# Performance work log

Hardware: AMD Instinct MI355X
Metric: run time of the kernel (lower is better)

The kernel has to match this reference:

```python
import jax, jax.numpy as jnp
import numpy as np

NEG_SLOPE = 0.2  # DenseGATConv default negative_slope


def _add_self_loops(adj):
    n = adj.shape[-1]
    idx = jnp.arange(n)
    return adj.at[:, idx, idx].set(1.0)


def dense_gat_conv(x, adj, W, att_src, att_dst, bias, concat):
    """PyG DenseGATConv forward (eval mode, add_loop=True).
    x: [B,N,F], adj: [B,N,N] (0/1), W: [F,H*C], att_*: [H,C], bias: [H*C] or [C]."""
    B, N, _ = x.shape
    H, C = att_src.shape
    h = (x @ W).reshape(B, N, H, C)                     # projected features
    a_src = jnp.einsum('bnhc,hc->bnh', h, att_src)      # [B,N,H]
    a_dst = jnp.einsum('bnhc,hc->bnh', h, att_dst)      # [B,N,H]
    # alpha[b,i,j,h] = a_src[b,j,h] + a_dst[b,i,h]
    alpha = a_src[:, None, :, :] + a_dst[:, :, None, :]  # [B,N,N,H]
    alpha = jax.nn.leaky_relu(alpha, NEG_SLOPE)
    adj = _add_self_loops(adj)
    alpha = jnp.where(adj[..., None] == 0, -jnp.inf, alpha)
    alpha = jax.nn.softmax(alpha, axis=2)               # softmax over sources j
    out = jnp.einsum('bijh,bjhc->bihc', alpha, h)       # [B,N,H,C]
    out = out.reshape(B, N, H * C) if concat else out.mean(axis=2)
    return out + bias


def setup_inputs() -> dict:
    key = jax.random.key(0)
    ks = jax.random.split(key, 10)
    B, N, F, H, C, NC = 1, 4096, 512, 8, 64, 16
    x = jax.random.normal(ks[0], (B, N, F), dtype=jnp.float32)
    adj = (jax.random.uniform(ks[1], (B, N, N)) < 0.01).astype(jnp.float32)
    s1 = 1.0 / np.sqrt(F)
    s2 = 1.0 / np.sqrt(H * C)
    return {
        'x': x,
        'adj': adj,
        'W1': jax.random.normal(ks[2], (F, H * C), dtype=jnp.float32) * s1,
        'att_src1': jax.random.normal(ks[3], (H, C), dtype=jnp.float32) * s1,
        'att_dst1': jax.random.normal(ks[4], (H, C), dtype=jnp.float32) * s1,
        'b1': jnp.zeros((H * C,), dtype=jnp.float32),
        'W2': jax.random.normal(ks[5], (H * C, NC), dtype=jnp.float32) * s2,
        'att_src2': jax.random.normal(ks[6], (1, NC), dtype=jnp.float32) * s2,
        'att_dst2': jax.random.normal(ks[7], (1, NC), dtype=jnp.float32) * s2,
        'b2': jnp.zeros((NC,), dtype=jnp.float32),
    }


def reference(x, adj, W1, att_src1, att_dst1, b1, W2, att_src2, att_dst2, b2):
    # eval mode: all dropout(p=0.6) layers are identity
    h = dense_gat_conv(x, adj, W1, att_src1, att_dst1, b1, concat=True)
    h = jax.nn.elu(h)
    out = dense_gat_conv(h, adj, W2, att_src2, att_dst2, b2, concat=False)
    return out
```

## Files before the change

### kernel.cpp

```cpp
#include <hip/hip_runtime.h>
#include <hip/hip_bf16.h>
#include <hip/hip_fp16.h>

#define N_NODES 4096
#define F_IN    512
#define HC      512
#define H_HEADS 8
#define C_DIM   64
#define NCLS    16
#define CAP     192
#define NEG_SLOPE 0.2f

typedef __bf16 bf16x8 __attribute__((ext_vector_type(8)));
typedef float  f32x4  __attribute__((ext_vector_type(4)));
typedef unsigned short us8 __attribute__((ext_vector_type(8)));


__global__ __launch_bounds__(256) void k_build_csr(const float* __restrict__ adj,
                                                   int* __restrict__ row_cnt,
                                                   int* __restrict__ col_idx) {
    int i = blockIdx.x;
    int t = threadIdx.x;
    __shared__ int cnt_s;
    if (t == 0) cnt_s = 0;
    __syncthreads();
    const float4* row = (const float4*)(adj + (size_t)i * N_NODES);
    int* cols = col_idx + (size_t)i * CAP;
#pragma unroll
    for (int it = 0; it < 4; ++it) {
        int idx4 = it * 256 + t;
        float4 v = row[idx4];
        int j0 = idx4 * 4;
        if (v.x != 0.f && j0 + 0 != i) { int p = atomicAdd(&cnt_s, 1); if (p < CAP - 1) cols[p] = j0 + 0; }
        if (v.y != 0.f && j0 + 1 != i) { int p = atomicAdd(&cnt_s, 1); if (p < CAP - 1) cols[p] = j0 + 1; }
        if (v.z != 0.f && j0 + 2 != i) { int p = atomicAdd(&cnt_s, 1); if (p < CAP - 1) cols[p] = j0 + 2; }
        if (v.w != 0.f && j0 + 3 != i) { int p = atomicAdd(&cnt_s, 1); if (p < CAP - 1) cols[p] = j0 + 3; }
    }
    __syncthreads();
    if (t == 0) {
        int p = min(cnt_s, CAP - 1);
        cols[p] = i;
        row_cnt[i] = p + 1;
    }
}

__global__ __launch_bounds__(256) void k_split_x(const float* __restrict__ x,
                                                 ushort* __restrict__ hi,
                                                 ushort* __restrict__ lo) {
    int tid = blockIdx.x * 256 + threadIdx.x;
    int rg = tid >> 10;
    int c  = tid & 1023;
    int kb = c >> 6;
    int l  = c & 63;
    int row = rg * 16 + (l & 15);
    int kbase = kb * 32 + (l >> 4) * 8;
    const float* src = &x[(size_t)row * F_IN + kbase];
    float4 v0 = *(const float4*)&src[0];
    float4 v1 = *(const float4*)&src[4];
    float f[8] = {v0.x, v0.y, v0.z, v0.w, v1.x, v1.y, v1.z, v1.w};
    us8 hv, lv;
#pragma unroll
    for (int u = 0; u < 8; ++u) {
        __bf16 h = (__bf16)f[u];
        __bf16 lo_ = (__bf16)(f[u] - (float)h);
        hv[u] = __builtin_bit_cast(unsigned short, h);
        lv[u] = __builtin_bit_cast(unsigned short, lo_);
    }
    *(us8*)&hi[(size_t)tid * 8] = hv;
    *(us8*)&lo[(size_t)tid * 8] = lv;
}

__global__ __launch_bounds__(256) void k_split_wT(const float* __restrict__ W,
                                                  ushort* __restrict__ hiT,
                                                  ushort* __restrict__ loT) {
    __shared__ float tile[64][65];
    int t = threadIdx.x;
    int n0 = blockIdx.x * 64, k0 = blockIdx.y * 64;
#pragma unroll
    for (int i = 0; i < 4; ++i) {
        int r = i * 16 + (t >> 4);
        int c = (t & 15) * 4;
        *(float4*)&tile[r][c] = *(const float4*)&W[(size_t)(k0 + r) * HC + n0 + c];
    }
    __syncthreads();
    int rg_local = t >> 6;
    int l = t & 63;
    int n_local = rg_local * 16 + (l & 15);
#pragma unroll
    for (int kb_local = 0; kb_local < 2; ++kb_local) {
        int k_local = kb_local * 32 + (l >> 4) * 8;
        us8 hv, lv;
#pragma unroll
        for (int u = 0; u < 8; ++u) {
            float f = tile[k_local + u][n_local];
            __bf16 h = (__bf16)f;
            __bf16 lo_ = (__bf16)(f - (float)h);
            hv[u] = __builtin_bit_cast(unsigned short, h);
            lv[u] = __builtin_bit_cast(unsigned short, lo_);
        }
        int rg = (n0 >> 4) + rg_local;
        int kb = (k0 >> 5) + kb_local;
        size_t off = ((size_t)(rg * 16 + kb) * 64 + l) * 8;
        *(us8*)&hiT[off] = hv;
        *(us8*)&loT[off] = lv;
    }
}

__global__ __launch_bounds__(256) void k_gemm1(const ushort* __restrict__ Ahi,
                                               const ushort* __restrict__ Alo,
                                               const ushort* __restrict__ Bhi,
                                               const ushort* __restrict__ Blo,
                                               __half* __restrict__ C) {
    __shared__ __align__(16) ushort smem[4][2048];
    int t = threadIdx.x;
    int w = t >> 6, lane = t & 63;
    int n0 = blockIdx.x * 64;
    int m0 = blockIdx.y * 64;
    const ushort* src = (w == 0) ? Ahi : (w == 1) ? Alo : (w == 2) ? Bhi : Blo;
    int rg0 = ((w < 2) ? m0 : n0) >> 4;
    int mw = (w & 1) * 32, nw = (w >> 1) * 32;
    f32x4 acc[2][2] = {};
    for (int kb = 0; kb < 16; ++kb) {
#pragma unroll
        for (int g = 0; g < 4; ++g) {
            const ushort* gp = src + ((size_t)((rg0 + g) * 16 + kb) * 64 + lane) * 8;
            __builtin_amdgcn_global_load_lds(
                (const __attribute__((address_space(1))) void*)gp,
                (__attribute__((address_space(3))) void*)&smem[w][g * 512],
                16, 0, 0);
        }
        __syncthreads();
        bf16x8 ahi[2], alo[2], bhi[2], blo[2];
#pragma unroll
        for (int mi = 0; mi < 2; ++mi) {
            int g = (mw >> 4) + mi;
            ahi[mi] = __builtin_bit_cast(bf16x8, *(const us8*)&smem[0][g * 512 + lane * 8]);
            alo[mi] = __builtin_bit_cast(bf16x8, *(const us8*)&smem[1][g * 512 + lane * 8]);
        }
#pragma unroll
        for (int ni = 0; ni < 2; ++ni) {
            int g = (nw >> 4) + ni;
            bhi[ni] = __builtin_bit_cast(bf16x8, *(const us8*)&smem[2][g * 512 + lane * 8]);
            blo[ni] = __builtin_bit_cast(bf16x8, *(const us8*)&smem[3][g * 512 + lane * 8]);
        }
#pragma unroll
        for (int mi = 0; mi < 2; ++mi)
#pragma unroll
            for (int ni = 0; ni < 2; ++ni) {
                acc[mi][ni] = __builtin_amdgcn_mfma_f32_16x16x32_bf16(ahi[mi], bhi[ni], acc[mi][ni], 0, 0, 0);
                acc[mi][ni] = __builtin_amdgcn_mfma_f32_16x16x32_bf16(alo[mi], bhi[ni], acc[mi][ni], 0, 0, 0);
                acc[mi][ni] = __builtin_amdgcn_mfma_f32_16x16x32_bf16(ahi[mi], blo[ni], acc[mi][ni], 0, 0, 0);
            }
        __syncthreads();
    }
    int r0 = (lane >> 4) * 4;
    int cn = lane & 15;
#pragma unroll
    for (int mi = 0; mi < 2; ++mi)
#pragma unroll
        for (int ni = 0; ni < 2; ++ni) {
            size_t base = (size_t)(m0 + mw + mi * 16 + r0) * HC + (n0 + nw + ni * 16 + cn);
#pragma unroll
            for (int r = 0; r < 4; ++r)
                C[base + (size_t)r * HC] = __float2half(acc[mi][ni][r]);
        }
}

__global__ __launch_bounds__(256) void k_attn1(const __half* __restrict__ hf,
                                               const float* __restrict__ att_src,
                                               const float* __restrict__ att_dst,
                                               float* __restrict__ a_src,
                                               float* __restrict__ a_dst) {
    int i = blockIdx.x;
    int t = threadIdx.x;
    int lane = t & 63;
    int w = t >> 6;
#pragma unroll
    for (int half = 0; half < 2; ++half) {
        int e = half * 256 + w * 64 + lane;
        float v = __half2float(hf[(size_t)i * HC + e]);
        float s = v * att_src[e];
        float d = v * att_dst[e];
#pragma unroll
        for (int o = 32; o > 0; o >>= 1) {
            s += __shfl_down(s, o, 64);
            d += __shfl_down(d, o, 64);
        }
        if (lane == 0) {
            int h = e >> 6;
            a_src[i * H_HEADS + h] = s;
            a_dst[i * H_HEADS + h] = d;
        }
    }
}

__global__ __launch_bounds__(256) void k_agg1(const __half* __restrict__ hf,
                                              const float* __restrict__ a_src,
                                              const float* __restrict__ a_dst,
                                              const int* __restrict__ row_cnt,
                                              const int* __restrict__ col_idx,
                                              const float* __restrict__ b1,
                                              float* __restrict__ elu1) {
    int i = blockIdx.x;
    int t = threadIdx.x;
    __shared__ float wL[CAP][H_HEADS];
    __shared__ int   colL[CAP];
    __shared__ float denom[H_HEADS];
    __shared__ float ad[H_HEADS];
    int cnt = row_cnt[i];
    if (t < H_HEADS) ad[t] = a_dst[i * H_HEADS + t];
    for (int j = t; j < cnt; j += 256) colL[j] = col_idx[(size_t)i * CAP + j];
    __syncthreads();
    for (int idx = t; idx < cnt * H_HEADS; idx += 256) {
        int j = idx >> 3, h = idx & 7;
        float l = a_src[colL[j] * H_HEADS + h] + ad[h];
        l = (l > 0.f) ? l : NEG_SLOPE * l;
        wL[j][h] = __expf(l);
    }
    __syncthreads();
    if (t < H_HEADS) {
        float s = 0.f;
        for (int j = 0; j < cnt; ++j) s += wL[j][t];
        denom[t] = s;
    }
    __syncthreads();
    int e = t * 2;
    int h = e >> 6;
    float ax = 0.f, ay = 0.f;
    int j = 0;
    for (; j + 4 <= cnt; j += 4) {
        int c0 = colL[j], c1 = colL[j + 1], c2 = colL[j + 2], c3 = colL[j + 3];
        float2 v0 = __half22float2(*(const __half2*)&hf[(size_t)c0 * HC + e]);
        float2 v1 = __half22float2(*(const __half2*)&hf[(size_t)c1 * HC + e]);
        float2 v2 = __half22float2(*(const __half2*)&hf[(size_t)c2 * HC + e]);
        float2 v3 = __half22float2(*(const __half2*)&hf[(size_t)c3 * HC + e]);
        float w0 = wL[j][h], w1 = wL[j + 1][h], w2 = wL[j + 2][h], w3 = wL[j + 3][h];
        ax += w0 * v0.x + w1 * v1.x + w2 * v2.x + w3 * v3.x;
        ay += w0 * v0.y + w1 * v1.y + w2 * v2.y + w3 * v3.y;
    }
    for (; j < cnt; ++j) {
        int c0 = colL[j];
        float2 v0 = __half22float2(*(const __half2*)&hf[(size_t)c0 * HC + e]);
        float w0 = wL[j][h];
        ax += w0 * v0.x;
        ay += w0 * v0.y;
    }
    float inv = 1.f / denom[h];
    float o0 = ax * inv + b1[e];
    float o1 = ay * inv + b1[e + 1];
    o0 = (o0 > 0.f) ? o0 : (__expf(o0) - 1.f);
    o1 = (o1 > 0.f) ? o1 : (__expf(o1) - 1.f);
    float2 ov = make_float2(o0, o1);
    *(float2*)&elu1[(size_t)i * HC + e] = ov;
}

__global__ __launch_bounds__(256) void k_gemm2(const float* __restrict__ elu1,
                                               const float* __restrict__ W2,
                                               const float* __restrict__ att_src2,
                                               const float* __restrict__ att_dst2,
                                               float* __restrict__ h2,
                                               float* __restrict__ a_src2,
                                               float* __restrict__ a_dst2) {
    __shared__ float W2s[HC * NCLS];
    __shared__ float h2s[16][NCLS];
    int t = threadIdx.x;
    int n0 = blockIdx.x * 16;
#pragma unroll
    for (int u = 0; u < 8; ++u) {
        int idx = (u * 256 + t) * 4;
        *(float4*)&W2s[idx] = *(const float4*)&W2[idx];
    }
    __syncthreads();
    int nl = t >> 4, c = t & 15;
    const float* row = elu1 + (size_t)(n0 + nl) * HC;
    float acc = 0.f;
    for (int k = 0; k < HC; k += 4) {
        float4 v = *(const float4*)&row[k];
        acc += v.x * W2s[(k + 0) * NCLS + c] + v.y * W2s[(k + 1) * NCLS + c]
             + v.z * W2s[(k + 2) * NCLS + c] + v.w * W2s[(k + 3) * NCLS + c];
    }
    h2[(size_t)(n0 + nl) * NCLS + c] = acc;
    h2s[nl][c] = acc;
    __syncthreads();
    if (t < 16) {
        float s = 0.f, d = 0.f;
#pragma unroll
        for (int cc = 0; cc < NCLS; ++cc) {
            s += h2s[t][cc] * att_src2[cc];
            d += h2s[t][cc] * att_dst2[cc];
        }
        a_src2[n0 + t] = s;
        a_dst2[n0 + t] = d;
    }
}

__global__ __launch_bounds__(256) void k_agg2(const float* __restrict__ h2,
                                              const float* __restrict__ a_src2,
                                              const float* __restrict__ a_dst2,
                                              const int* __restrict__ row_cnt,
                                              const int* __restrict__ col_idx,
                                              const float* __restrict__ b2,
                                              float* __restrict__ out) {
    int t = threadIdx.x;
    int w = t >> 6, lane = t & 63;
    int i = blockIdx.x * 4 + w;
    __shared__ float ew[4][CAP];
    __shared__ int   colL[4][CAP];
    int cnt = row_cnt[i];
    float adi = a_dst2[i];
    float sum = 0.f;
    for (int j = lane; j < cnt; j += 64) {
        int col = col_idx[(size_t)i * CAP + j];
        colL[w][j] = col;
        float l = a_src2[col] + adi;
        l = (l > 0.f) ? l : NEG_SLOPE * l;
        float e = __expf(l);
        ew[w][j] = e;
        sum += e;
    }
#pragma unroll
    for (int o = 32; o > 0; o >>= 1) sum += __shfl_xor(sum, o, 64);
    int q = lane >> 4, c = lane & 15;
    float acc = 0.f;
    for (int j = q; j < cnt; j += 4)
        acc += ew[w][j] * h2[(size_t)colL[w][j] * NCLS + c];
    acc += __shfl_down(acc, 32, 64);
    acc += __shfl_down(acc, 16, 64);
    if (lane < NCLS)
        out[(size_t)i * NCLS + lane] = acc / sum + b2[lane];
}

extern "C" void kernel_launch(void* const* d_in, const int* in_sizes, int n_in,
                              void* d_out, int out_size, void* d_ws, size_t ws_size,
                              hipStream_t stream) {
    const float* x        = (const float*)d_in[0];
    const float* adj      = (const float*)d_in[1];
    const float* W1       = (const float*)d_in[2];
    const float* att_src1 = (const float*)d_in[3];
    const float* att_dst1 = (const float*)d_in[4];
    const float* b1       = (const float*)d_in[5];
    const float* W2       = (const float*)d_in[6];
    const float* att_src2 = (const float*)d_in[7];
    const float* att_dst2 = (const float*)d_in[8];
    const float* b2       = (const float*)d_in[9];
    float* out = (float*)d_out;

    char* ws = (char*)d_ws;
    int*    row_cnt = (int*)ws;     ws += (size_t)N_NODES * 4;
    int*    col_idx = (int*)ws;     ws += (size_t)N_NODES * CAP * 4;
    __half* h1f     = (__half*)ws;  ws += (size_t)N_NODES * HC * 2;
    float*  a_src   = (float*)ws;   ws += (size_t)N_NODES * H_HEADS * 4;
    float*  a_dst   = (float*)ws;   ws += (size_t)N_NODES * H_HEADS * 4;
    float*  elu1    = (float*)ws;   ws += (size_t)N_NODES * HC * 4;
    float*  h2      = (float*)ws;   ws += (size_t)N_NODES * NCLS * 4;
    float*  as2     = (float*)ws;   ws += (size_t)N_NODES * 4;
    float*  ad2     = (float*)ws;   ws += (size_t)N_NODES * 4;
    ushort* x_hi    = (ushort*)ws;  ws += (size_t)N_NODES * F_IN * 2;
    ushort* x_lo    = (ushort*)ws;  ws += (size_t)N_NODES * F_IN * 2;
    ushort* w_hiT   = (ushort*)ws;  ws += (size_t)F_IN * HC * 2;
    ushort* w_loT   = (ushort*)ws;  ws += (size_t)F_IN * HC * 2;

    hipLaunchKernelGGL(k_split_x, dim3(N_NODES * F_IN / (256 * 8)), dim3(256), 0, stream, x, x_hi, x_lo);
    hipLaunchKernelGGL(k_split_wT, dim3(8, 8), dim3(256), 0, stream, W1, w_hiT, w_loT);
    hipLaunchKernelGGL(k_build_csr, dim3(N_NODES), dim3(256), 0, stream, adj, row_cnt, col_idx);
    hipLaunchKernelGGL(k_gemm1, dim3(HC / 64, N_NODES / 64), dim3(256), 0, stream, x_hi, x_lo, w_hiT, w_loT, h1f);
    hipLaunchKernelGGL(k_attn1, dim3(N_NODES), dim3(256), 0, stream, h1f, att_src1, att_dst1, a_src, a_dst);
    hipLaunchKernelGGL(k_agg1, dim3(N_NODES), dim3(256), 0, stream, h1f, a_src, a_dst, row_cnt, col_idx, b1, elu1);
    hipLaunchKernelGGL(k_gemm2, dim3(N_NODES / 16), dim3(256), 0, stream, elu1, W2, att_src2, att_dst2, h2, as2, ad2);
    hipLaunchKernelGGL(k_agg2, dim3(N_NODES / 4), dim3(256), 0, stream, h2, as2, ad2, row_cnt, col_idx, b2, out);
}
```

Baseline: 172.0 us.

## Merge prep kernels, fuse attention logits into GEMM epilogue, store ELU output in fp16

Merges the x split, W split and CSR build into one launch that dispatches on block index, cutting launch count. Computes the per-head attention logits inside the first GEMM epilogue with lane shuffles and shared-memory reduction, which removes the separate attn1 kernel and its re-read of h1. Stores the layer-1 ELU output as fp16 to halve that write and its re-read in gemm2, and parallelises the softmax denominator sum across 32 lanes per head. The fp16 intermediate adds rounding error to the second layer's input.

```diff
diff --git a/kernel.cpp b/kernel.cpp
--- a/kernel.cpp
+++ b/kernel.cpp
@@ -16,93 +16,98 @@
 typedef unsigned short us8 __attribute__((ext_vector_type(8)));
 
 
-__global__ __launch_bounds__(256) void k_build_csr(const float* __restrict__ adj,
-                                                   int* __restrict__ row_cnt,
-                                                   int* __restrict__ col_idx) {
-    int i = blockIdx.x;
-    int t = threadIdx.x;
+#define XBLKS 1024
+#define WBLKS 64
+
+__global__ __launch_bounds__(256) void k_prep(const float* __restrict__ x,
+                                              const float* __restrict__ W,
+                                              const float* __restrict__ adj,
+                                              ushort* __restrict__ xhi,
+                                              ushort* __restrict__ xlo,
+                                              ushort* __restrict__ whiT,
+                                              ushort* __restrict__ wloT,
+                                              int* __restrict__ row_cnt,
+                                              int* __restrict__ col_idx) {
+    __shared__ float tile[64][65];
     __shared__ int cnt_s;
-    if (t == 0) cnt_s = 0;
-    __syncthreads();
-    const float4* row = (const float4*)(adj + (size_t)i * N_NODES);
-    int* cols = col_idx + (size_t)i * CAP;
-#pragma unroll
-    for (int it = 0; it < 4; ++it) {
-        int idx4 = it * 256 + t;
-        float4 v = row[idx4];
-        int j0 = idx4 * 4;
-        if (v.x != 0.f && j0 + 0 != i) { int p = atomicAdd(&cnt_s, 1); if (p < CAP - 1) cols[p] = j0 + 0; }
-        if (v.y != 0.f && j0 + 1 != i) { int p = atomicAdd(&cnt_s, 1); if (p < CAP - 1) cols[p] = j0 + 1; }
-        if (v.z != 0.f && j0 + 2 != i) { int p = atomicAdd(&cnt_s, 1); if (p < CAP - 1) cols[p] = j0 + 2; }
-        if (v.w != 0.f && j0 + 3 != i) { int p = atomicAdd(&cnt_s, 1); if (p < CAP - 1) cols[p] = j0 + 3; }
-    }
-    __syncthreads();
-    if (t == 0) {
-        int p = min(cnt_s, CAP - 1);
-        cols[p] = i;
-        row_cnt[i] = p + 1;
-    }
-}
-
-__global__ __launch_bounds__(256) void k_split_x(const float* __restrict__ x,
-                                                 ushort* __restrict__ hi,
-                                                 ushort* __restrict__ lo) {
-    int tid = blockIdx.x * 256 + threadIdx.x;
-    int rg = tid >> 10;
-    int c  = tid & 1023;
-    int kb = c >> 6;
-    int l  = c & 63;
-    int row = rg * 16 + (l & 15);
-    int kbase = kb * 32 + (l >> 4) * 8;
-    const float* src = &x[(size_t)row * F_IN + kbase];
-    float4 v0 = *(const float4*)&src[0];
-    float4 v1 = *(const float4*)&src[4];
-    float f[8] = {v0.x, v0.y, v0.z, v0.w, v1.x, v1.y, v1.z, v1.w};
-    us8 hv, lv;
-#pragma unroll
-    for (int u = 0; u < 8; ++u) {
-        __bf16 h = (__bf16)f[u];
-        __bf16 lo_ = (__bf16)(f[u] - (float)h);
-        hv[u] = __builtin_bit_cast(unsigned short, h);
-        lv[u] = __builtin_bit_cast(unsigned short, lo_);
-    }
-    *(us8*)&hi[(size_t)tid * 8] = hv;
-    *(us8*)&lo[(size_t)tid * 8] = lv;
-}
-
-__global__ __launch_bounds__(256) void k_split_wT(const float* __restrict__ W,
-                                                  ushort* __restrict__ hiT,
-                                                  ushort* __restrict__ loT) {
-    __shared__ float tile[64][65];
-    int t = threadIdx.x;
-    int n0 = blockIdx.x * 64, k0 = blockIdx.y * 64;
-#pragma unroll
-    for (int i = 0; i < 4; ++i) {
-        int r = i * 16 + (t >> 4);
-        int c = (t & 15) * 4;
-        *(float4*)&tile[r][c] = *(const float4*)&W[(size_t)(k0 + r) * HC + n0 + c];
-    }
-    __syncthreads();
-    int rg_local = t >> 6;
-    int l = t & 63;
-    int n_local = rg_local * 16 + (l & 15);
-#pragma unroll
-    for (int kb_local = 0; kb_local < 2; ++kb_local) {
-        int k_local = kb_local * 32 + (l >> 4) * 8;
+    int b = blockIdx.x;
+    int t = threadIdx.x;
+    if (b < XBLKS) {
+        int tid = b * 256 + t;
+        int rg = tid >> 9;
+        rg = tid >> 10;
+        int c  = tid & 1023;
+        int kb = c >> 6;
+        int l  = c & 63;
+        int row = rg * 16 + (l & 15);
+        int kbase = kb * 32 + (l >> 4) * 8;
+        const float* src = &x[(size_t)row * F_IN + kbase];
+        float4 v0 = *(const float4*)&src[0];
+        float4 v1 = *(const float4*)&src[4];
+        float f[8] = {v0.x, v0.y, v0.z, v0.w, v1.x, v1.y, v1.z, v1.w};
         us8 hv, lv;
 #pragma unroll
         for (int u = 0; u < 8; ++u) {
-            float f = tile[k_local + u][n_local];
-            __bf16 h = (__bf16)f;
-            __bf16 lo_ = (__bf16)(f - (float)h);
+            __bf16 h = (__bf16)f[u];
+            __bf16 lo_ = (__bf16)(f[u] - (float)h);
             hv[u] = __builtin_bit_cast(unsigned short, h);
             lv[u] = __builtin_bit_cast(unsigned short, lo_);
         }
-        int rg = (n0 >> 4) + rg_local;
-        int kb = (k0 >> 5) + kb_local;
-        size_t off = ((size_t)(rg * 16 + kb) * 64 + l) * 8;
-        *(us8*)&hiT[off] = hv;
-        *(us8*)&loT[off] = lv;
+        *(us8*)&xhi[(size_t)tid * 8] = hv;
+        *(us8*)&xlo[(size_t)tid * 8] = lv;
+    } else if (b < XBLKS + WBLKS) {
+        int bb = b - XBLKS;
+        int n0 = (bb & 7) * 64, k0 = (bb >> 3) * 64;
+#pragma unroll
+        for (int i = 0; i < 4; ++i) {
+            int r = i * 16 + (t >> 4);
+            int c = (t & 15) * 4;
+            *(float4*)&tile[r][c] = *(const float4*)&W[(size_t)(k0 + r) * HC + n0 + c];
+        }
+        __syncthreads();
+        int rg_local = t >> 6;
+        int l = t & 63;
+        int n_local = rg_local * 16 + (l & 15);
+#pragma unroll
+        for (int kb_local = 0; kb_local < 2; ++kb_local) {
+            int k_local = kb_local * 32 + (l >> 4) * 8;
+            us8 hv, lv;
+#pragma unroll
+            for (int u = 0; u < 8; ++u) {
+                float f = tile[k_local + u][n_local];
+                __bf16 h = (__bf16)f;
+                __bf16 lo_ = (__bf16)(f - (float)h);
+                hv[u] = __builtin_bit_cast(unsigned short, h);
+                lv[u] = __builtin_bit_cast(unsigned short, lo_);
+            }
+            int rg = (n0 >> 4) + rg_local;
+            int kb = (k0 >> 5) + kb_local;
+            size_t off = ((size_t)(rg * 16 + kb) * 64 + l) * 8;
+            *(us8*)&whiT[off] = hv;
+            *(us8*)&wloT[off] = lv;
+        }
+    } else {
+        int i = b - (XBLKS + WBLKS);
+        if (t == 0) cnt_s = 0;
+        __syncthreads();
+        const float4* row = (const float4*)(adj + (size_t)i * N_NODES);
+        int* cols = col_idx + (size_t)i * CAP;
+#pragma unroll
+        for (int it = 0; it < 4; ++it) {
+            int idx4 = it * 256 + t;
+            float4 v = row[idx4];
+            int j0 = idx4 * 4;
+            if (v.x != 0.f && j0 + 0 != i) { int p = atomicAdd(&cnt_s, 1); if (p < CAP - 1) cols[p] = j0 + 0; }
+            if (v.y != 0.f && j0 + 1 != i) { int p = atomicAdd(&cnt_s, 1); if (p < CAP - 1) cols[p] = j0 + 1; }
+            if (v.z != 0.f && j0 + 2 != i) { int p = atomicAdd(&cnt_s, 1); if (p < CAP - 1) cols[p] = j0 + 2; }
+            if (v.w != 0.f && j0 + 3 != i) { int p = atomicAdd(&cnt_s, 1); if (p < CAP - 1) cols[p] = j0 + 3; }
+        }
+        __syncthreads();
+        if (t == 0) {
+            int p = min(cnt_s, CAP - 1);
+            cols[p] = i;
+            row_cnt[i] = p + 1;
+        }
     }
 }
 
@@ -110,8 +115,13 @@
                                                const ushort* __restrict__ Alo,
                                                const ushort* __restrict__ Bhi,
                                                const ushort* __restrict__ Blo,
-                                               __half* __restrict__ C) {
+                                               const float* __restrict__ att_src,
+                                               const float* __restrict__ att_dst,
+                                               __half* __restrict__ C,
+                                               float* __restrict__ a_src,
+                                               float* __restrict__ a_dst) {
     __shared__ __align__(16) ushort smem[4][2048];
+    __shared__ float s_s[2][64], s_d[2][64];
     int t = threadIdx.x;
     int w = t >> 6, lane = t & 63;
     int n0 = blockIdx.x * 64;
@@ -155,6 +165,25 @@
     }
     int r0 = (lane >> 4) * 4;
     int cn = lane & 15;
+    float as0 = att_src[n0 + nw + cn],      as1 = att_src[n0 + nw + 16 + cn];
+    float ad0 = att_dst[n0 + nw + cn],      ad1 = att_dst[n0 + nw + 16 + cn];
+#pragma unroll
+    for (int mi = 0; mi < 2; ++mi)
+#pragma unroll
+        for (int r = 0; r < 4; ++r) {
+            float ps = acc[mi][0][r] * as0 + acc[mi][1][r] * as1;
+            float pd = acc[mi][0][r] * ad0 + acc[mi][1][r] * ad1;
+#pragma unroll
+            for (int o = 1; o < 16; o <<= 1) {
+                ps += __shfl_xor(ps, o, 64);
+                pd += __shfl_xor(pd, o, 64);
+            }
+            if (cn == 0) {
+                int row = mw + mi * 16 + r0 + r;
+                s_s[w >> 1][row] = ps;
+                s_d[w >> 1][row] = pd;
+            }
+        }
 #pragma unroll
     for (int mi = 0; mi < 2; ++mi)
 #pragma unroll
@@ -164,33 +193,10 @@
             for (int r = 0; r < 4; ++r)
                 C[base + (size_t)r * HC] = __float2half(acc[mi][ni][r]);
         }
-}
-
-__global__ __launch_bounds__(256) void k_attn1(const __half* __restrict__ hf,
-                                               const float* __restrict__ att_src,
-                                               const float* __restrict__ att_dst,
-                                               float* __restrict__ a_src,
-                                               float* __restrict__ a_dst) {
-    int i = blockIdx.x;
-    int t = threadIdx.x;
-    int lane = t & 63;
-    int w = t >> 6;
-#pragma unroll
-    for (int half = 0; half < 2; ++half) {
-        int e = half * 256 + w * 64 + lane;
-        float v = __half2float(hf[(size_t)i * HC + e]);
-        float s = v * att_src[e];
-        float d = v * att_dst[e];
-#pragma unroll
-        for (int o = 32; o > 0; o >>= 1) {
-            s += __shfl_down(s, o, 64);
-            d += __shfl_down(d, o, 64);
-        }
-        if (lane == 0) {
-            int h = e >> 6;
-            a_src[i * H_HEADS + h] = s;
-            a_dst[i * H_HEADS + h] = d;
-        }
+    __syncthreads();
+    if (t < 64) {
+        a_src[(m0 + t) * H_HEADS + blockIdx.x] = s_s[0][t] + s_s[1][t];
+        a_dst[(m0 + t) * H_HEADS + blockIdx.x] = s_d[0][t] + s_d[1][t];
     }
 }
 
@@ -200,7 +206,7 @@
                                               const int* __restrict__ row_cnt,
                                               const int* __restrict__ col_idx,
                                               const float* __restrict__ b1,
-                                              float* __restrict__ elu1) {
+                                              __half* __restrict__ elu1) {
     int i = blockIdx.x;
     int t = threadIdx.x;
     __shared__ float wL[CAP][H_HEADS];
@@ -218,10 +224,13 @@
         wL[j][h] = __expf(l);
     }
     __syncthreads();
-    if (t < H_HEADS) {
+    {
+        int h = t >> 5, l32 = t & 31;
         float s = 0.f;
-        for (int j = 0; j < cnt; ++j) s += wL[j][t];
-        denom[t] = s;
+        for (int j = l32; j < cnt; j += 32) s += wL[j][h];
+#pragma unroll
+        for (int o = 16; o > 0; o >>= 1) s += __shfl_down(s, o, 32);
+        if (l32 == 0) denom[h] = s;
     }
     __syncthreads();
     int e = t * 2;
@@ -250,11 +259,10 @@
     float o1 = ay * inv + b1[e + 1];
     o0 = (o0 > 0.f) ? o0 : (__expf(o0) - 1.f);
     o1 = (o1 > 0.f) ? o1 : (__expf(o1) - 1.f);
-    float2 ov = make_float2(o0, o1);
-    *(float2*)&elu1[(size_t)i * HC + e] = ov;
-}
-
-__global__ __launch_bounds__(256) void k_gemm2(const float* __restrict__ elu1,
+    *(__half2*)&elu1[(size_t)i * HC + e] = __floats2half2_rn(o0, o1);
+}
+
+__global__ __launch_bounds__(256) void k_gemm2(const __half* __restrict__ elu1,
                                                const float* __restrict__ W2,
                                                const float* __restrict__ att_src2,
                                                const float* __restrict__ att_dst2,
@@ -272,12 +280,13 @@
     }
     __syncthreads();
     int nl = t >> 4, c = t & 15;
-    const float* row = elu1 + (size_t)(n0 + nl) * HC;
+    const __half2* row = (const __half2*)(elu1 + (size_t)(n0 + nl) * HC);
     float acc = 0.f;
     for (int k = 0; k < HC; k += 4) {
-        float4 v = *(const float4*)&row[k];
-        acc += v.x * W2s[(k + 0) * NCLS + c] + v.y * W2s[(k + 1) * NCLS + c]
-             + v.z * W2s[(k + 2) * NCLS + c] + v.w * W2s[(k + 3) * NCLS + c];
+        float2 v0 = __half22float2(row[k >> 1]);
+        float2 v1 = __half22float2(row[(k >> 1) + 1]);
+        acc += v0.x * W2s[(k + 0) * NCLS + c] + v0.y * W2s[(k + 1) * NCLS + c]
+             + v1.x * W2s[(k + 2) * NCLS + c] + v1.y * W2s[(k + 3) * NCLS + c];
     }
     h2[(size_t)(n0 + nl) * NCLS + c] = acc;
     h2s[nl][c] = acc;
@@ -351,7 +360,7 @@
     __half* h1f     = (__half*)ws;  ws += (size_t)N_NODES * HC * 2;
     float*  a_src   = (float*)ws;   ws += (size_t)N_NODES * H_HEADS * 4;
     float*  a_dst   = (float*)ws;   ws += (size_t)N_NODES * H_HEADS * 4;
-    float*  elu1    = (float*)ws;   ws += (size_t)N_NODES * HC * 4;
+    __half* elu1    = (__half*)ws;  ws += (size_t)N_NODES * HC * 2;
     float*  h2      = (float*)ws;   ws += (size_t)N_NODES * NCLS * 4;
     float*  as2     = (float*)ws;   ws += (size_t)N_NODES * 4;
     float*  ad2     = (float*)ws;   ws += (size_t)N_NODES * 4;
@@ -360,12 +369,14 @@
     ushort* w_hiT   = (ushort*)ws;  ws += (size_t)F_IN * HC * 2;
     ushort* w_loT   = (ushort*)ws;  ws += (size_t)F_IN * HC * 2;
 
-    hipLaunchKernelGGL(k_split_x, dim3(N_NODES * F_IN / (256 * 8)), dim3(256), 0, stream, x, x_hi, x_lo);
-    hipLaunchKernelGGL(k_split_wT, dim3(8, 8), dim3(256), 0, stream, W1, w_hiT, w_loT);
-    hipLaunchKernelGGL(k_build_csr, dim3(N_NODES), dim3(256), 0, stream, adj, row_cnt, col_idx);
-    hipLaunchKernelGGL(k_gemm1, dim3(HC / 64, N_NODES / 64), dim3(256), 0, stream, x_hi, x_lo, w_hiT, w_loT, h1f);
-    hipLaunchKernelGGL(k_attn1, dim3(N_NODES), dim3(256), 0, stream, h1f, att_src1, att_dst1, a_src, a_dst);
-    hipLaunchKernelGGL(k_agg1, dim3(N_NODES), dim3(256), 0, stream, h1f, a_src, a_dst, row_cnt, col_idx, b1, elu1);
-    hipLaunchKernelGGL(k_gemm2, dim3(N_NODES / 16), dim3(256), 0, stream, elu1, W2, att_src2, att_dst2, h2, as2, ad2);
-    hipLaunchKernelGGL(k_agg2, dim3(N_NODES / 4), dim3(256), 0, stream, h2, as2, ad2, row_cnt, col_idx, b2, out);
-}
+    hipLaunchKernelGGL(k_prep, dim3(XBLKS + WBLKS + N_NODES), dim3(256), 0, stream,
+                       x, W1, adj, x_hi, x_lo, w_hiT, w_loT, row_cnt, col_idx);
+    hipLaunchKernelGGL(k_gemm1, dim3(HC / 64, N_NODES / 64), dim3(256), 0, stream,
+                       x_hi, x_lo, w_hiT, w_loT, att_src1, att_dst1, h1f, a_src, a_dst);
+    hipLaunchKernelGGL(k_agg1, dim3(N_NODES), dim3(256), 0, stream,
+                       h1f, a_src, a_dst, row_cnt, col_idx, b1, elu1);
+    hipLaunchKernelGGL(k_gemm2, dim3(N_NODES / 16), dim3(256), 0, stream,
+                       elu1, W2, att_src2, att_dst2, h2, as2, ad2);
+    hipLaunchKernelGGL(k_agg2, dim3(N_NODES / 4), dim3(256), 0, stream,
+                       h2, as2, ad2, row_cnt, col_idx, b2, out);
+}
```

Result: faster. 165.2 us (-3.9%).
